# Kernel tuning notes

Hardware: AMD Instinct MI355X
Metric: run time of the kernel (lower is better)

Reference implementation:

```python
import jax, jax.numpy as jnp
import numpy as np
from jax import lax

B, C, H, W = 8, 128, 48, 48
N = H * W
SPARSITY = 0.8
K_TOP = int(N * SPARSITY)


def conv2d(x, w, b, padding, dilation=1):
    # x: [B,C,H,W], w: [O,I,kh,kw]
    out = lax.conv_general_dilated(
        x, w, window_strides=(1, 1),
        padding=[(padding, padding), (padding, padding)],
        rhs_dilation=(dilation, dilation),
        dimension_numbers=('NCHW', 'OIHW', 'NCHW'))
    return out + b[None, :, None, None]


def setup_inputs() -> dict:
    key = jax.random.key(0)
    ks = jax.random.split(key, 16)
    s = 0.02
    return {
        'x': jax.random.normal(ks[0], (B, C, H, W), jnp.float32),
        'prev_features': jax.random.normal(ks[1], (B, C, H, W), jnp.float32),
        'Wq': jax.random.normal(ks[2], (C, C), jnp.float32) * s,
        'bq': jnp.zeros((C,), jnp.float32),
        'Wk': jax.random.normal(ks[3], (C, C), jnp.float32) * s,
        'bk': jnp.zeros((C,), jnp.float32),
        'Wv': jax.random.normal(ks[4], (C, C), jnp.float32) * s,
        'bv': jnp.zeros((C,), jnp.float32),
        'ref_w': jax.random.normal(ks[5], (C, C, 3, 3), jnp.float32) * s,
        'ref_b': jnp.zeros((C,), jnp.float32),
        'gate_w': jax.random.normal(ks[6], (1, C, 3, 3), jnp.float32) * s,
        'gate_b': jnp.zeros((1,), jnp.float32),
        'cov_w': jax.random.normal(ks[7], (C, C, 3, 3), jnp.float32) * s,
        'cov_b': jnp.zeros((C,), jnp.float32),
    }


def reference(x, prev_features, Wq, bq, Wk, bk, Wv, bv,
              ref_w, ref_b, gate_w, gate_b, cov_w, cov_b):
    b_, c_, h_, w_ = x.shape
    n_ = h_ * w_
    # torch x.view(B, -1, C): raw reshape of NCHW memory (NOT a transpose)
    t = x.reshape(b_, n_, c_)
    # Linear layers (torch: y = x @ W.T + b)
    Q = t @ Wq.T + bq
    Kt = (t @ Wk.T + bk).transpose(0, 2, 1)  # [B,C,N]
    V = t @ Wv.T + bv
    attn = jnp.einsum('bnc,bcm->bnm', Q, Kt) / (c_ ** 0.5)  # [B,N,N]
    # top-k masking with scatter, as in the original
    _, idx = lax.top_k(attn, K_TOP)  # [B,N,k]
    bi = jnp.arange(b_)[:, None, None]
    ni = jnp.arange(n_)[None, :, None]
    mask = jnp.zeros_like(attn).at[bi, ni, idx].set(1.0)
    attn = attn * mask - 1e10 * (1.0 - mask)
    attn = jax.nn.softmax(attn, axis=-1)
    out = jnp.einsum('bnm,bmc->bnc', attn, V)  # [B,N,C]
    # torch view([B, C, sqrt(N), sqrt(N)]): raw reshape
    xs = out.reshape(b_, c_, h_, w_)
    # localized refinement
    importance = jax.nn.sigmoid(conv2d(xs, gate_w, gate_b, padding=1))
    xr = conv2d(xs * importance, ref_w, ref_b, padding=1)
    xs = xs + xr
    # temporal propagation
    xs = xs + 0.5 * prev_features
    # fast coverage conv: kernel 3, dilation 2, padding = 1 + 2 - 1 = 2
    return conv2d(xs, cov_w, cov_b, padding=2, dilation=2)
```

## Files before the change

kernel.cpp:

```cpp
#include <hip/hip_runtime.h>
#include <hip/hip_bf16.h>
#include <math.h>

#define BB 8
#define CC 128
#define NTOK 2304
#define KTOP 1843

typedef unsigned short u16;
typedef unsigned int   u32;
typedef __attribute__((ext_vector_type(8))) short short8;
typedef __attribute__((ext_vector_type(4))) float f32x4;

static __device__ __forceinline__ float bf2f(u16 u) {
    return __uint_as_float(((u32)u) << 16);
}
static __device__ __forceinline__ u16 f2bf(float f) {
    u32 x = __float_as_uint(f);
    return (u16)((x + 0x7fffu + ((x >> 16) & 1u)) >> 16);
}
static __device__ __forceinline__ float key2val(int k) {
    u32 raw = (k & 0x8000) ? (u32)(k ^ 0x8000) : ((~(u32)k) & 0xFFFFu);
    return __uint_as_float(raw << 16);
}

__global__ __launch_bounds__(256) void qkv_kernel(
    const float* __restrict__ x,
    const float* __restrict__ Wq, const float* __restrict__ bq,
    const float* __restrict__ Wk, const float* __restrict__ bk,
    const float* __restrict__ Wv, const float* __restrict__ bv,
    u16* __restrict__ q_ws, u16* __restrict__ k_ws, u16* __restrict__ v_ws)
{
    __shared__ float t_lds[128 * 68];
    __shared__ u16 st[64 * 128];
    int blk = blockIdx.x;
    int b  = blk / 36;
    int n0 = (blk % 36) * 64;
    int tid = threadIdx.x;
    const float* xb = x + (size_t)(b * NTOK + n0) * CC;
    #pragma unroll
    for (int k = 0; k < 32; ++k) {
        int idx = k * 256 + tid;
        t_lds[(idx & 127) * 68 + (idx >> 7)] = xb[idx];
    }
    __syncthreads();
    int o  = tid & 127;
    int rh = tid >> 7;
    const float* Ws[3] = {Wq, Wk, Wv};
    const float* bs[3] = {bq, bk, bv};
    for (int mat = 0; mat < 3; ++mat) {
        const float* W = Ws[mat];
        float acc[32];
        #pragma unroll
        for (int j = 0; j < 32; ++j) acc[j] = 0.f;
        for (int c = 0; c < 128; ++c) {
            float w = W[o * 128 + c];
            const float4* t4p = (const float4*)&t_lds[c * 68 + rh * 32];
            #pragma unroll
            for (int j4 = 0; j4 < 8; ++j4) {
                float4 t4 = t4p[j4];
                acc[j4*4+0] += t4.x * w;
                acc[j4*4+1] += t4.y * w;
                acc[j4*4+2] += t4.z * w;
                acc[j4*4+3] += t4.w * w;
            }
        }
        float bias = bs[mat][o];
        if (mat == 2) {
            ushort4* vp4 = (ushort4*)(v_ws + (size_t)(b * CC + o) * NTOK + n0 + rh * 32);
            #pragma unroll
            for (int j8 = 0; j8 < 8; ++j8) {
                ushort4 s;
                s.x = f2bf(acc[j8*4+0] + bias); s.y = f2bf(acc[j8*4+1] + bias);
                s.z = f2bf(acc[j8*4+2] + bias); s.w = f2bf(acc[j8*4+3] + bias);
                vp4[j8] = s;
            }
        } else {
            float sc = (mat == 0) ? 0.08838834764831845f : 1.0f;
            #pragma unroll
            for (int j = 0; j < 32; ++j)
                st[(rh * 32 + j) * 128 + o] = f2bf((acc[j] + bias) * sc);
            __syncthreads();
            u16* gp = (mat == 0 ? q_ws : k_ws) + (size_t)(b * NTOK + n0) * CC;
            const ushort4* s4 = (const ushort4*)st;
            ushort4* g4 = (ushort4*)gp;
            for (int k = tid; k < 2048; k += 256) g4[k] = s4[k];
            __syncthreads();
        }
    }
}

__global__ __launch_bounds__(256) void attn_kernel(
    const u16* __restrict__ q_ws, const u16* __restrict__ k_ws,
    const u16* __restrict__ v_ws, float* __restrict__ xs_ws)
{
    __shared__ u16 sp[8 * NTOK];
    __shared__ float rowinv[8];
    int tid  = threadIdx.x;
    int lane = tid & 63, wid = tid >> 6;
    int b  = blockIdx.x & 7;
    int n0 = (blockIdx.x >> 3) * 8;
    int fr = lane & 15;
    int fg = lane >> 4;

    const u16* qbase = q_ws + (size_t)(b * NTOK + n0 + (fr & 7)) * CC + fg * 8;
    short8 qa[4];
    #pragma unroll
    for (int kc = 0; kc < 4; ++kc)
        qa[kc] = *(const short8*)(qbase + kc * 32);

    const u16* kb = k_ws + (size_t)(b * NTOK + fr) * CC + fg * 8;
    for (int t = wid; t < 144; t += 4) {
        int m0 = t * 16;
        f32x4 acc = {0.f, 0.f, 0.f, 0.f};
        const u16* kp = kb + (size_t)m0 * CC;
        #pragma unroll
        for (int kc = 0; kc < 4; ++kc) {
            short8 kf = *(const short8*)(kp + kc * 32);
            acc = __builtin_amdgcn_mfma_f32_16x16x32_bf16(qa[kc], kf, acc, 0, 0, 0);
        }
        if (fg < 2) {
            int mcol = m0 + fr;
            #pragma unroll
            for (int r = 0; r < 4; ++r) {
                int q = fg * 4 + r;
                u16 raw = f2bf(acc[r]);
                u16 key = (raw & 0x8000u) ? (u16)~raw : (u16)(raw | 0x8000u);
                sp[q * NTOK + (mcol ^ ((q & 7) << 3))] = key;
            }
        }
    }
    __syncthreads();

    {
        int row0 = wid * 2, row1 = row0 + 1;
        int x0 = (row0 & 7) << 3, x1 = (row1 & 7) << 3;
        u16* s0 = sp + row0 * NTOK;
        u16* s1 = sp + row1 * NTOK;
        int keys0[36], keys1[36];
        int kmax0 = 0, kmax1 = 0;
        #pragma unroll
        for (int j = 0; j < 36; ++j) {
            int m = lane + j * 64;
            int k0 = s0[m ^ x0];
            int k1 = s1[m ^ x1];
            keys0[j] = k0; keys1[j] = k1;
            kmax0 = max(kmax0, k0); kmax1 = max(kmax1, k1);
        }
        #pragma unroll
        for (int off = 32; off; off >>= 1) {
            kmax0 = max(kmax0, __shfl_xor(kmax0, off, 64));
            kmax1 = max(kmax1, __shfl_xor(kmax1, off, 64));
        }
        u32 res0 = 0, res1 = 0;
        for (int bit = 15; bit >= 0; --bit) {
            int cand0 = (int)(res0 | (1u << bit));
            int cand1 = (int)(res1 | (1u << bit));
            int c0 = 0, c1 = 0;
            #pragma unroll
            for (int j = 0; j < 36; ++j) {
                c0 += (keys0[j] >= cand0) ? 1 : 0;
                c1 += (keys1[j] >= cand1) ? 1 : 0;
            }
            #pragma unroll
            for (int off = 32; off; off >>= 1) {
                c0 += __shfl_xor(c0, off, 64);
                c1 += __shfl_xor(c1, off, 64);
            }
            if (c0 >= KTOP) res0 = (u32)cand0;
            if (c1 >= KTOP) res1 = (u32)cand1;
        }
        float vmax0 = key2val(kmax0), vmax1 = key2val(kmax1);
        float sum0 = 0.f, sum1 = 0.f;
        #pragma unroll
        for (int j = 0; j < 36; ++j) {
            int m = lane + j * 64;
            float e0 = 0.f, e1 = 0.f;
            if ((u32)keys0[j] >= res0) e0 = __expf(key2val(keys0[j]) - vmax0);
            if ((u32)keys1[j] >= res1) e1 = __expf(key2val(keys1[j]) - vmax1);
            s0[m ^ x0] = f2bf(e0);
            s1[m ^ x1] = f2bf(e1);
            sum0 += e0; sum1 += e1;
        }
        #pragma unroll
        for (int off = 32; off; off >>= 1) {
            sum0 += __shfl_xor(sum0, off, 64);
            sum1 += __shfl_xor(sum1, off, 64);
        }
        if (lane == 0) {
            rowinv[row0] = 1.f / sum0;
            rowinv[row1] = 1.f / sum1;
        }
    }
    __syncthreads();

    {
        int c0 = wid * 32;
        const u16* arow = sp + (fr & 7) * NTOK;
        int xorv = (fr & 7) << 3;
        const u16* vb0 = v_ws + (size_t)(b * CC + c0 + fr) * NTOK + fg * 8;
        const u16* vb1 = vb0 + (size_t)16 * NTOK;
        f32x4 oa = {0.f, 0.f, 0.f, 0.f};
        f32x4 ob = {0.f, 0.f, 0.f, 0.f};
        for (int ch = 0; ch < 72; ++ch) {
            int m0 = ch * 32;
            short8 pa = *(const short8*)(arow + ((m0 + fg * 8) ^ xorv));
            short8 v0 = *(const short8*)(vb0 + m0);
            short8 v1 = *(const short8*)(vb1 + m0);
            oa = __builtin_amdgcn_mfma_f32_16x16x32_bf16(pa, v0, oa, 0, 0, 0);
            ob = __builtin_amdgcn_mfma_f32_16x16x32_bf16(pa, v1, ob, 0, 0, 0);
        }
        if (fg < 2) {
            #pragma unroll
            for (int r = 0; r < 4; ++r) {
                int q = fg * 4 + r;
                float inv = rowinv[q];
                size_t base = (size_t)(b * NTOK + n0 + q) * CC + c0;
                xs_ws[base + fr]      = oa[r] * inv;
                xs_ws[base + 16 + fr] = ob[r] * inv;
            }
        }
    }
}

__global__ __launch_bounds__(256) void gate_kernel(
    const float* __restrict__ xs_ws, const float* __restrict__ gw,
    const float* __restrict__ gb, float* __restrict__ imp_ws)
{
    __shared__ float gsum[256];
    int blk = blockIdx.x;
    int b  = blk & 7;
    int p0 = (blk >> 3) * 64;
    int tid = threadIdx.x;
    int pl = tid & 63, cq = tid >> 6;
    int p = p0 + pl;
    int h = p / 48, w = p % 48;
    float acc = 0.f;
    const float* xb = xs_ws + (size_t)b * CC * NTOK;
    for (int i = cq * 32; i < cq * 32 + 32; ++i) {
        const float* plane = xb + (size_t)i * NTOK;
        const float* wv = gw + i * 9;
        #pragma unroll
        for (int kh = 0; kh < 3; ++kh) {
            int hh = h + kh - 1;
            if ((unsigned)hh >= 48u) continue;
            #pragma unroll
            for (int kw = 0; kw < 3; ++kw) {
                int ww = w + kw - 1;
                if ((unsigned)ww >= 48u) continue;
                acc += plane[hh * 48 + ww] * wv[kh * 3 + kw];
            }
        }
    }
    gsum[cq * 64 + pl] = acc;
    __syncthreads();
    if (tid < 64) {
        float s = gsum[tid] + gsum[64 + tid] + gsum[128 + tid] + gsum[192 + tid] + gb[0];
        imp_ws[b * NTOK + p0 + tid] = 1.f / (1.f + __expf(-s));
    }
}

__global__ __launch_bounds__(256) void wtrans_kernel(
    const float* __restrict__ rw, const float* __restrict__ cw,
    u16* __restrict__ wb_ref, u16* __restrict__ wb_cov)
{
    int idx = blockIdx.x * 256 + threadIdx.x;
    int which = idx >= 147456;
    int rem = which ? idx - 147456 : idx;
    int tap = rem >> 14;
    int rest = rem & 16383;
    int o = rest >> 7, c = rest & 127;
    const float* src = which ? cw : rw;
    u16* dst = which ? wb_cov : wb_ref;
    dst[rem] = f2bf(src[(o * 128 + c) * 9 + tap]);
}

__global__ __launch_bounds__(256) void tpos_kernel(
    const float* __restrict__ xs_ws, const float* __restrict__ prev,
    const float* __restrict__ imp_ws,
    u16* __restrict__ xt_g, float* __restrict__ rbuf)
{
    __shared__ float tx[128 * 65];
    __shared__ float tp[128 * 65];
    int blk = blockIdx.x;
    int b  = blk & 7;
    int p0 = (blk >> 3) * 64;
    int tid = threadIdx.x;
    const float* xsb = xs_ws + (size_t)b * CC * NTOK + p0;
    const float* pvb = prev  + (size_t)b * CC * NTOK + p0;
    #pragma unroll
    for (int it = 0; it < 32; ++it) {
        int idx = it * 256 + tid;
        int i = idx >> 6, pp = idx & 63;
        tx[i * 65 + pp] = xsb[(size_t)i * NTOK + pp];
        tp[i * 65 + pp] = pvb[(size_t)i * NTOK + pp];
    }
    __syncthreads();
    int pl = tid & 63, cq = tid >> 6;
    float impv = imp_ws[b * NTOK + p0 + pl];
    size_t obase = ((size_t)b * NTOK + p0 + pl) * CC + cq * 32;
    u16* gout = xt_g + obase;
    float* rout = rbuf + obase;
    #pragma unroll
    for (int j4 = 0; j4 < 8; ++j4) {
        float4 rv; ushort4 gv;
        float v0 = tx[(cq * 32 + j4 * 4 + 0) * 65 + pl];
        float v1 = tx[(cq * 32 + j4 * 4 + 1) * 65 + pl];
        float v2 = tx[(cq * 32 + j4 * 4 + 2) * 65 + pl];
        float v3 = tx[(cq * 32 + j4 * 4 + 3) * 65 + pl];
        float q0 = tp[(cq * 32 + j4 * 4 + 0) * 65 + pl];
        float q1 = tp[(cq * 32 + j4 * 4 + 1) * 65 + pl];
        float q2 = tp[(cq * 32 + j4 * 4 + 2) * 65 + pl];
        float q3 = tp[(cq * 32 + j4 * 4 + 3) * 65 + pl];
        rv.x = v0 + 0.5f * q0; rv.y = v1 + 0.5f * q1;
        rv.z = v2 + 0.5f * q2; rv.w = v3 + 0.5f * q3;
        gv.x = f2bf(v0 * impv); gv.y = f2bf(v1 * impv);
        gv.z = f2bf(v2 * impv); gv.w = f2bf(v3 * impv);
        *(float4*)(rout + j4 * 4) = rv;
        *(ushort4*)(gout + j4 * 4) = gv;
    }
}

__global__ __launch_bounds__(256) void refgemm_kernel(
    const u16* __restrict__ xt_g, const u16* __restrict__ wb_ref,
    const float* __restrict__ rbuf, const float* __restrict__ rb,
    u16* __restrict__ xt2)
{
    __shared__ u16 slab[144 * 128];
    int tid = threadIdx.x;
    int lane = tid & 63, wid = tid >> 6;
    int blk = blockIdx.x;
    int b  = blk & 7;
    int st = (blk >> 3) & 15;
    int oh = blk >> 7;
    int h0 = st * 3;
    int p0g = st * 144;
    int fr = lane & 15, fg = lane >> 4;
    int o0 = oh * 64 + wid * 16;
    const u16* xb = xt_g + (size_t)b * NTOK * CC;

    f32x4 acc[9];
    #pragma unroll
    for (int pt = 0; pt < 9; ++pt) acc[pt] = (f32x4){0.f, 0.f, 0.f, 0.f};

    for (int tap = 0; tap < 9; ++tap) {
        int dh = tap / 3 - 1, dw = tap % 3 - 1;
        __syncthreads();
        #pragma unroll
        for (int it = 0; it < 9; ++it) {
            int idx = it * 256 + tid;
            int pr = idx >> 4, cv = idx & 15;
            int r = pr >= 96 ? 2 : (pr >= 48 ? 1 : 0);
            int w = pr - r * 48;
            int sh = h0 + r + dh, sw = w + dw;
            short8 val = (short8){0,0,0,0,0,0,0,0};
            if ((unsigned)sh < 48u && (unsigned)sw < 48u)
                val = *(const short8*)(xb + (size_t)(sh * 48 + sw) * CC + cv * 8);
            *(short8*)(slab + pr * 128 + ((cv ^ (pr & 7)) * 8)) = val;
        }
        __syncthreads();
        #pragma unroll
        for (int kc = 0; kc < 4; ++kc) {
            short8 bfr = *(const short8*)(wb_ref + tap * 16384 + (o0 + fr) * 128 + kc * 32 + fg * 8);
            #pragma unroll
            for (int pt = 0; pt < 9; ++pt) {
                int prr = pt * 16 + fr;
                short8 pa = *(const short8*)(slab + prr * 128 + (((kc * 4 + fg) ^ (prr & 7)) * 8));
                acc[pt] = __builtin_amdgcn_mfma_f32_16x16x32_bf16(pa, bfr, acc[pt], 0, 0, 0);
            }
        }
    }
    int o = o0 + fr;
    float bias = rb[o];
    #pragma unroll
    for (int pt = 0; pt < 9; ++pt) {
        #pragma unroll
        for (int r = 0; r < 4; ++r) {
            int p = p0g + pt * 16 + fg * 4 + r;
            size_t off = ((size_t)b * NTOK + p) * CC + o;
            float v = acc[pt][r] + bias + rbuf[off];
            xt2[off] = f2bf(v);
        }
    }
}

__global__ __launch_bounds__(256) void covgemm_kernel(
    const u16* __restrict__ xt2, const u16* __restrict__ wb_cov,
    const float* __restrict__ cb, float* __restrict__ out)
{
    __shared__ u16 slab[144 * 128];
    __shared__ float ldsout[4 * 16 * 145];
    int tid = threadIdx.x;
    int lane = tid & 63, wid = tid >> 6;
    int blk = blockIdx.x;
    int b  = blk & 7;
    int st = (blk >> 3) & 15;
    int oh = blk >> 7;
    int h0 = st * 3;
    int p0g = st * 144;
    int fr = lane & 15, fg = lane >> 4;
    int o0 = oh * 64 + wid * 16;
    const u16* xb = xt2 + (size_t)b * NTOK * CC;

    f32x4 acc[9];
    #pragma unroll
    for (int pt = 0; pt < 9; ++pt) acc[pt] = (f32x4){0.f, 0.f, 0.f, 0.f};

    for (int tap = 0; tap < 9; ++tap) {
        int dh = (tap / 3 - 1) * 2, dw = (tap % 3 - 1) * 2;
        __syncthreads();
        #pragma unroll
        for (int it = 0; it < 9; ++it) {
            int idx = it * 256 + tid;
            int pr = idx >> 4, cv = idx & 15;
            int r = pr >= 96 ? 2 : (pr >= 48 ? 1 : 0);
            int w = pr - r * 48;
            int sh = h0 + r + dh, sw = w + dw;
            short8 val = (short8){0,0,0,0,0,0,0,0};
            if ((unsigned)sh < 48u && (unsigned)sw < 48u)
                val = *(const short8*)(xb + (size_t)(sh * 48 + sw) * CC + cv * 8);
            *(short8*)(slab + pr * 128 + ((cv ^ (pr & 7)) * 8)) = val;
        }
        __syncthreads();
        #pragma unroll
        for (int kc = 0; kc < 4; ++kc) {
            short8 bfr = *(const short8*)(wb_cov + tap * 16384 + (o0 + fr) * 128 + kc * 32 + fg * 8);
            #pragma unroll
            for (int pt = 0; pt < 9; ++pt) {
                int prr = pt * 16 + fr;
                short8 pa = *(const short8*)(slab + prr * 128 + (((kc * 4 + fg) ^ (prr & 7)) * 8));
                acc[pt] = __builtin_amdgcn_mfma_f32_16x16x32_bf16(pa, bfr, acc[pt], 0, 0, 0);
            }
        }
    }
    float bias = cb[o0 + fr];
    float* lo = ldsout + wid * (16 * 145);
    #pragma unroll
    for (int pt = 0; pt < 9; ++pt) {
        #pragma unroll
        for (int r = 0; r < 4; ++r) {
            int pl = pt * 16 + fg * 4 + r;
            lo[fr * 145 + pl] = acc[pt][r] + bias;
        }
    }
    __syncthreads();
    float* ob = out + ((size_t)b * CC + o0) * NTOK + p0g;
    #pragma unroll
    for (int j = 0; j < 36; ++j) {
        int idx = j * 64 + lane;
        int o_r = idx / 144;
        int p_r = idx - o_r * 144;
        ob[(size_t)o_r * NTOK + p_r] = lo[o_r * 145 + p_r];
    }
}

extern "C" void kernel_launch(void* const* d_in, const int* in_sizes, int n_in,
                              void* d_out, int out_size, void* d_ws, size_t ws_size,
                              hipStream_t stream)
{
    const float* x    = (const float*)d_in[0];
    const float* prev = (const float*)d_in[1];
    const float* Wq   = (const float*)d_in[2];
    const float* bq   = (const float*)d_in[3];
    const float* Wk   = (const float*)d_in[4];
    const float* bk   = (const float*)d_in[5];
    const float* Wv   = (const float*)d_in[6];
    const float* bv   = (const float*)d_in[7];
    const float* rw   = (const float*)d_in[8];
    const float* rb   = (const float*)d_in[9];
    const float* gw   = (const float*)d_in[10];
    const float* gb   = (const float*)d_in[11];
    const float* cw   = (const float*)d_in[12];
    const float* cb   = (const float*)d_in[13];
    float* out = (float*)d_out;
    char* ws = (char*)d_ws;

    const size_t SZ  = (size_t)BB * NTOK * CC;
    const size_t BSZ = SZ * 2;
    const size_t FSZ = SZ * 4;
    u16*   q_ws   = (u16*)(ws);
    u16*   k_ws   = (u16*)(ws + BSZ);
    u16*   v_ws   = (u16*)(ws + 2 * BSZ);
    float* xs_ws  = (float*)(ws + 3 * BSZ);
    float* imp_ws = (float*)(ws + 3 * BSZ + FSZ);
    u16*   xt_g   = (u16*)(ws + 3 * BSZ + FSZ + 73728);
    float* rbuf   = (float*)(ws + 4 * BSZ + FSZ + 73728);
    u16*   xt2    = (u16*)(ws + 4 * BSZ + 2 * FSZ + 73728);
    u16*   wb_ref = (u16*)(ws + 5 * BSZ + 2 * FSZ + 73728);
    u16*   wb_cov = (u16*)(ws + 5 * BSZ + 2 * FSZ + 73728 + 294912);

    qkv_kernel<<<dim3(288), dim3(256), 0, stream>>>(x, Wq, bq, Wk, bk, Wv, bv,
                                                    q_ws, k_ws, v_ws);
    attn_kernel<<<dim3(2304), dim3(256), 0, stream>>>(q_ws, k_ws, v_ws, xs_ws);
    gate_kernel<<<dim3(288), dim3(256), 0, stream>>>(xs_ws, gw, gb, imp_ws);
    wtrans_kernel<<<dim3(1152), dim3(256), 0, stream>>>(rw, cw, wb_ref, wb_cov);
    tpos_kernel<<<dim3(288), dim3(256), 0, stream>>>(xs_ws, prev, imp_ws, xt_g, rbuf);
    refgemm_kernel<<<dim3(256), dim3(256), 0, stream>>>(xt_g, wb_ref, rbuf, rb, xt2);
    covgemm_kernel<<<dim3(256), dim3(256), 0, stream>>>(xt2, wb_cov, cb, out);
}
```

Baseline: 656.2 us.

## Split fused attention into QK, top-k softmax, and PV kernels via global scores

Replaces the single fused attention kernel, which kept an 8-row score slab in LDS, with three kernels. The first writes the full bf16 score matrix to global memory using 64x64 tiles, the second does the per-row radix top-k and softmax in place, and the third does the PV GEMM with 32-row by 64-channel tiles. The aim is to avoid the fused kernel's low MFMA utilisation and large LDS footprint, and to tile K and V better. The cost is about 85MB of score traffic written and read several times, plus extra launches.

New measurement: 570.1 us. 1.15x faster.

```diff
diff --git a/kernel.cpp b/kernel.cpp
--- a/kernel.cpp
+++ b/kernel.cpp
@@ -90,136 +90,156 @@
     }
 }
 
-__global__ __launch_bounds__(256) void attn_kernel(
+__global__ __launch_bounds__(256) void qk_kernel(
     const u16* __restrict__ q_ws, const u16* __restrict__ k_ws,
-    const u16* __restrict__ v_ws, float* __restrict__ xs_ws)
-{
-    __shared__ u16 sp[8 * NTOK];
-    __shared__ float rowinv[8];
-    int tid  = threadIdx.x;
+    u16* __restrict__ sc)
+{
+    int tid = threadIdx.x;
     int lane = tid & 63, wid = tid >> 6;
-    int b  = blockIdx.x & 7;
-    int n0 = (blockIdx.x >> 3) * 8;
-    int fr = lane & 15;
-    int fg = lane >> 4;
-
-    const u16* qbase = q_ws + (size_t)(b * NTOK + n0 + (fr & 7)) * CC + fg * 8;
+    int blk = blockIdx.x;
+    int b = blk & 7;
+    int t = blk >> 3;
+    int qt = t % 36, mt = t / 36;
+    int q0 = qt * 64 + wid * 16;
+    int m0 = mt * 64;
+    int fr = lane & 15, fg = lane >> 4;
+
+    const u16* qb = q_ws + (size_t)(b * NTOK + q0 + fr) * CC + fg * 8;
     short8 qa[4];
     #pragma unroll
-    for (int kc = 0; kc < 4; ++kc)
-        qa[kc] = *(const short8*)(qbase + kc * 32);
-
-    const u16* kb = k_ws + (size_t)(b * NTOK + fr) * CC + fg * 8;
-    for (int t = wid; t < 144; t += 4) {
-        int m0 = t * 16;
-        f32x4 acc = {0.f, 0.f, 0.f, 0.f};
-        const u16* kp = kb + (size_t)m0 * CC;
+    for (int kc = 0; kc < 4; ++kc) qa[kc] = *(const short8*)(qb + kc * 32);
+
+    const u16* kb = k_ws + (size_t)(b * NTOK + m0 + fr) * CC + fg * 8;
+    f32x4 acc[4];
+    #pragma unroll
+    for (int i = 0; i < 4; ++i) acc[i] = (f32x4){0.f, 0.f, 0.f, 0.f};
+    #pragma unroll
+    for (int mt2 = 0; mt2 < 4; ++mt2) {
+        const u16* kp = kb + (size_t)(mt2 * 16) * CC;
         #pragma unroll
         for (int kc = 0; kc < 4; ++kc) {
             short8 kf = *(const short8*)(kp + kc * 32);
-            acc = __builtin_amdgcn_mfma_f32_16x16x32_bf16(qa[kc], kf, acc, 0, 0, 0);
-        }
-        if (fg < 2) {
-            int mcol = m0 + fr;
-            #pragma unroll
-            for (int r = 0; r < 4; ++r) {
-                int q = fg * 4 + r;
-                u16 raw = f2bf(acc[r]);
-                u16 key = (raw & 0x8000u) ? (u16)~raw : (u16)(raw | 0x8000u);
-                sp[q * NTOK + (mcol ^ ((q & 7) << 3))] = key;
-            }
-        }
-    }
-    __syncthreads();
-
-    {
-        int row0 = wid * 2, row1 = row0 + 1;
-        int x0 = (row0 & 7) << 3, x1 = (row1 & 7) << 3;
-        u16* s0 = sp + row0 * NTOK;
-        u16* s1 = sp + row1 * NTOK;
-        int keys0[36], keys1[36];
-        int kmax0 = 0, kmax1 = 0;
+            acc[mt2] = __builtin_amdgcn_mfma_f32_16x16x32_bf16(qa[kc], kf, acc[mt2], 0, 0, 0);
+        }
+    }
+    #pragma unroll
+    for (int mt2 = 0; mt2 < 4; ++mt2) {
+        #pragma unroll
+        for (int r = 0; r < 4; ++r) {
+            int row = q0 + fg * 4 + r;
+            int col = m0 + mt2 * 16 + fr;
+            u16 raw = f2bf(acc[mt2][r]);
+            u16 key = (raw & 0x8000u) ? (u16)~raw : (u16)(raw | 0x8000u);
+            sc[((size_t)b * NTOK + row) * NTOK + col] = key;
+        }
+    }
+}
+
+__global__ __launch_bounds__(256) void topk_kernel(
+    u16* __restrict__ sc, float* __restrict__ rowinv)
+{
+    int tid = threadIdx.x;
+    int lane = tid & 63, wid = tid >> 6;
+    size_t rg0 = (size_t)blockIdx.x * 8 + wid * 2;
+    u16* s0 = sc + rg0 * NTOK;
+    u16* s1 = s0 + NTOK;
+
+    int keys0[36], keys1[36];
+    int kmax0 = 0, kmax1 = 0;
+    #pragma unroll
+    for (int j = 0; j < 9; ++j) {
+        ushort4 a = *(const ushort4*)(s0 + j * 256 + lane * 4);
+        ushort4 c = *(const ushort4*)(s1 + j * 256 + lane * 4);
+        keys0[j*4+0] = a.x; keys0[j*4+1] = a.y; keys0[j*4+2] = a.z; keys0[j*4+3] = a.w;
+        keys1[j*4+0] = c.x; keys1[j*4+1] = c.y; keys1[j*4+2] = c.z; keys1[j*4+3] = c.w;
+        kmax0 = max(kmax0, max(max((int)a.x, (int)a.y), max((int)a.z, (int)a.w)));
+        kmax1 = max(kmax1, max(max((int)c.x, (int)c.y), max((int)c.z, (int)c.w)));
+    }
+    #pragma unroll
+    for (int off = 32; off; off >>= 1) {
+        kmax0 = max(kmax0, __shfl_xor(kmax0, off, 64));
+        kmax1 = max(kmax1, __shfl_xor(kmax1, off, 64));
+    }
+    u32 res0 = 0, res1 = 0;
+    for (int bit = 15; bit >= 0; --bit) {
+        int cand0 = (int)(res0 | (1u << bit));
+        int cand1 = (int)(res1 | (1u << bit));
+        int c0 = 0, c1 = 0;
         #pragma unroll
         for (int j = 0; j < 36; ++j) {
-            int m = lane + j * 64;
-            int k0 = s0[m ^ x0];
-            int k1 = s1[m ^ x1];
-            keys0[j] = k0; keys1[j] = k1;
-            kmax0 = max(kmax0, k0); kmax1 = max(kmax1, k1);
+            c0 += (keys0[j] >= cand0) ? 1 : 0;
+            c1 += (keys1[j] >= cand1) ? 1 : 0;
         }
         #pragma unroll
         for (int off = 32; off; off >>= 1) {
-            kmax0 = max(kmax0, __shfl_xor(kmax0, off, 64));
-            kmax1 = max(kmax1, __shfl_xor(kmax1, off, 64));
-        }
-        u32 res0 = 0, res1 = 0;
-        for (int bit = 15; bit >= 0; --bit) {
-            int cand0 = (int)(res0 | (1u << bit));
-            int cand1 = (int)(res1 | (1u << bit));
-            int c0 = 0, c1 = 0;
-            #pragma unroll
-            for (int j = 0; j < 36; ++j) {
-                c0 += (keys0[j] >= cand0) ? 1 : 0;
-                c1 += (keys1[j] >= cand1) ? 1 : 0;
-            }
-            #pragma unroll
-            for (int off = 32; off; off >>= 1) {
-                c0 += __shfl_xor(c0, off, 64);
-                c1 += __shfl_xor(c1, off, 64);
-            }
-            if (c0 >= KTOP) res0 = (u32)cand0;
-            if (c1 >= KTOP) res1 = (u32)cand1;
-        }
-        float vmax0 = key2val(kmax0), vmax1 = key2val(kmax1);
-        float sum0 = 0.f, sum1 = 0.f;
-        #pragma unroll
-        for (int j = 0; j < 36; ++j) {
-            int m = lane + j * 64;
-            float e0 = 0.f, e1 = 0.f;
-            if ((u32)keys0[j] >= res0) e0 = __expf(key2val(keys0[j]) - vmax0);
-            if ((u32)keys1[j] >= res1) e1 = __expf(key2val(keys1[j]) - vmax1);
-            s0[m ^ x0] = f2bf(e0);
-            s1[m ^ x1] = f2bf(e1);
-            sum0 += e0; sum1 += e1;
-        }
-        #pragma unroll
-        for (int off = 32; off; off >>= 1) {
-            sum0 += __shfl_xor(sum0, off, 64);
-            sum1 += __shfl_xor(sum1, off, 64);
-        }
-        if (lane == 0) {
-            rowinv[row0] = 1.f / sum0;
-            rowinv[row1] = 1.f / sum1;
-        }
-    }
-    __syncthreads();
-
-    {
-        int c0 = wid * 32;
-        const u16* arow = sp + (fr & 7) * NTOK;
-        int xorv = (fr & 7) << 3;
-        const u16* vb0 = v_ws + (size_t)(b * CC + c0 + fr) * NTOK + fg * 8;
-        const u16* vb1 = vb0 + (size_t)16 * NTOK;
-        f32x4 oa = {0.f, 0.f, 0.f, 0.f};
-        f32x4 ob = {0.f, 0.f, 0.f, 0.f};
-        for (int ch = 0; ch < 72; ++ch) {
-            int m0 = ch * 32;
-            short8 pa = *(const short8*)(arow + ((m0 + fg * 8) ^ xorv));
-            short8 v0 = *(const short8*)(vb0 + m0);
-            short8 v1 = *(const short8*)(vb1 + m0);
-            oa = __builtin_amdgcn_mfma_f32_16x16x32_bf16(pa, v0, oa, 0, 0, 0);
-            ob = __builtin_amdgcn_mfma_f32_16x16x32_bf16(pa, v1, ob, 0, 0, 0);
-        }
-        if (fg < 2) {
-            #pragma unroll
-            for (int r = 0; r < 4; ++r) {
-                int q = fg * 4 + r;
-                float inv = rowinv[q];
-                size_t base = (size_t)(b * NTOK + n0 + q) * CC + c0;
-                xs_ws[base + fr]      = oa[r] * inv;
-                xs_ws[base + 16 + fr] = ob[r] * inv;
-            }
-        }
+            c0 += __shfl_xor(c0, off, 64);
+            c1 += __shfl_xor(c1, off, 64);
+        }
+        if (c0 >= KTOP) res0 = (u32)cand0;
+        if (c1 >= KTOP) res1 = (u32)cand1;
+    }
+    float vmax0 = key2val(kmax0), vmax1 = key2val(kmax1);
+    float sum0 = 0.f, sum1 = 0.f;
+    #pragma unroll
+    for (int j = 0; j < 9; ++j) {
+        ushort4 w0, w1;
+        float e;
+        e = ((u32)keys0[j*4+0] >= res0) ? __expf(key2val(keys0[j*4+0]) - vmax0) : 0.f; sum0 += e; w0.x = f2bf(e);
+        e = ((u32)keys0[j*4+1] >= res0) ? __expf(key2val(keys0[j*4+1]) - vmax0) : 0.f; sum0 += e; w0.y = f2bf(e);
+        e = ((u32)keys0[j*4+2] >= res0) ? __expf(key2val(keys0[j*4+2]) - vmax0) : 0.f; sum0 += e; w0.z = f2bf(e);
+        e = ((u32)keys0[j*4+3] >= res0) ? __expf(key2val(keys0[j*4+3]) - vmax0) : 0.f; sum0 += e; w0.w = f2bf(e);
+        e = ((u32)keys1[j*4+0] >= res1) ? __expf(key2val(keys1[j*4+0]) - vmax1) : 0.f; sum1 += e; w1.x = f2bf(e);
+        e = ((u32)keys1[j*4+1] >= res1) ? __expf(key2val(keys1[j*4+1]) - vmax1) : 0.f; sum1 += e; w1.y = f2bf(e);
+        e = ((u32)keys1[j*4+2] >= res1) ? __expf(key2val(keys1[j*4+2]) - vmax1) : 0.f; sum1 += e; w1.z = f2bf(e);
+        e = ((u32)keys1[j*4+3] >= res1) ? __expf(key2val(keys1[j*4+3]) - vmax1) : 0.f; sum1 += e; w1.w = f2bf(e);
+        *(ushort4*)(s0 + j * 256 + lane * 4) = w0;
+        *(ushort4*)(s1 + j * 256 + lane * 4) = w1;
+    }
+    #pragma unroll
+    for (int off = 32; off; off >>= 1) {
+        sum0 += __shfl_xor(sum0, off, 64);
+        sum1 += __shfl_xor(sum1, off, 64);
+    }
+    if (lane == 0) {
+        rowinv[rg0]     = 1.f / sum0;
+        rowinv[rg0 + 1] = 1.f / sum1;
+    }
+}
+
+__global__ __launch_bounds__(256) void pv_kernel(
+    const u16* __restrict__ sc, const u16* __restrict__ v_ws,
+    const float* __restrict__ rowinv, float* __restrict__ xs_ws)
+{
+    int tid = threadIdx.x;
+    int lane = tid & 63, wid = tid >> 6;
+    int blk = blockIdx.x;
+    int b = blk & 7;
+    int rt = blk >> 3;
+    int r0 = rt * 32 + (wid & 1) * 16;
+    int c0 = (wid >> 1) * 64;
+    int fr = lane & 15, fg = lane >> 4;
+
+    const u16* pb = sc + ((size_t)b * NTOK + r0 + fr) * NTOK + fg * 8;
+    const u16* vb = v_ws + (size_t)(b * CC + c0 + fr) * NTOK + fg * 8;
+    f32x4 acc[4];
+    #pragma unroll
+    for (int i = 0; i < 4; ++i) acc[i] = (f32x4){0.f, 0.f, 0.f, 0.f};
+    for (int ch = 0; ch < 72; ++ch) {
+        int m0 = ch * 32;
+        short8 pa = *(const short8*)(pb + m0);
+        #pragma unroll
+        for (int t = 0; t < 4; ++t) {
+            short8 vf = *(const short8*)(vb + (size_t)t * 16 * NTOK + m0);
+            acc[t] = __builtin_amdgcn_mfma_f32_16x16x32_bf16(pa, vf, acc[t], 0, 0, 0);
+        }
+    }
+    #pragma unroll
+    for (int r = 0; r < 4; ++r) {
+        int row = r0 + fg * 4 + r;
+        float inv = rowinv[(size_t)b * NTOK + row];
+        float* op = xs_ws + ((size_t)b * NTOK + row) * CC + c0;
+        #pragma unroll
+        for (int t = 0; t < 4; ++t) op[t * 16 + fr] = acc[t][r] * inv;
     }
 }
 
@@ -478,20 +498,27 @@
     const size_t SZ  = (size_t)BB * NTOK * CC;
     const size_t BSZ = SZ * 2;
     const size_t FSZ = SZ * 4;
+    const size_t SCB = (size_t)BB * NTOK * NTOK * 2;
+    const size_t RIB = (size_t)BB * NTOK * 4;
+
     u16*   q_ws   = (u16*)(ws);
     u16*   k_ws   = (u16*)(ws + BSZ);
     u16*   v_ws   = (u16*)(ws + 2 * BSZ);
-    float* xs_ws  = (float*)(ws + 3 * BSZ);
-    float* imp_ws = (float*)(ws + 3 * BSZ + FSZ);
-    u16*   xt_g   = (u16*)(ws + 3 * BSZ + FSZ + 73728);
-    float* rbuf   = (float*)(ws + 4 * BSZ + FSZ + 73728);
-    u16*   xt2    = (u16*)(ws + 4 * BSZ + 2 * FSZ + 73728);
-    u16*   wb_ref = (u16*)(ws + 5 * BSZ + 2 * FSZ + 73728);
-    u16*   wb_cov = (u16*)(ws + 5 * BSZ + 2 * FSZ + 73728 + 294912);
+    u16*   sc_ws  = (u16*)(ws + 3 * BSZ);
+    float* ri_ws  = (float*)(ws + 3 * BSZ + SCB);
+    float* xs_ws  = (float*)(ws + 3 * BSZ + SCB + RIB);
+    float* imp_ws = (float*)(ws + 3 * BSZ + SCB + RIB + FSZ);
+    u16*   xt_g   = (u16*)(ws + 3 * BSZ + SCB + 2 * RIB + FSZ);
+    float* rbuf   = (float*)(ws + 4 * BSZ + SCB + 2 * RIB + FSZ);
+    u16*   xt2    = (u16*)(ws + 4 * BSZ + SCB + 2 * RIB + 2 * FSZ);
+    u16*   wb_ref = (u16*)(ws + 5 * BSZ + SCB + 2 * RIB + 2 * FSZ);
+    u16*   wb_cov = (u16*)(ws + 5 * BSZ + SCB + 2 * RIB + 2 * FSZ + 294912);
 
     qkv_kernel<<<dim3(288), dim3(256), 0, stream>>>(x, Wq, bq, Wk, bk, Wv, bv,
                                                     q_ws, k_ws, v_ws);
-    attn_kernel<<<dim3(2304), dim3(256), 0, stream>>>(q_ws, k_ws, v_ws, xs_ws);
+    qk_kernel<<<dim3(10368), dim3(256), 0, stream>>>(q_ws, k_ws, sc_ws);
+    topk_kernel<<<dim3(2304), dim3(256), 0, stream>>>(sc_ws, ri_ws);
+    pv_kernel<<<dim3(576), dim3(256), 0, stream>>>(sc_ws, v_ws, ri_ws, xs_ws);
     gate_kernel<<<dim3(288), dim3(256), 0, stream>>>(xs_ws, gw, gb, imp_ws);
     wtrans_kernel<<<dim3(1152), dim3(256), 0, stream>>>(rw, cw, wb_ref, wb_cov);
     tpos_kernel<<<dim3(288), dim3(256), 0, stream>>>(xs_ws, prev, imp_ws, xt_g, rbuf);
```
